# Performance work log

Measured on AMD Instinct MI355X. Metric: run time of the kernel, lower is better.

The kernel has to match this reference:

```python
import jax, jax.numpy as jnp
import numpy as np

B, C_IN, H, W = 2, 32, 512, 512
HIDDEN, SIZE = 768, 16
LATENT, NUM_CLASS = 128, 21
HP, WP = H // SIZE, W // SIZE
EPS = 1e-8
TEMP = 0.5


def setup_inputs() -> dict:
    key = jax.random.key(0)
    k1, k2, k3, k4, k5 = jax.random.split(key, 5)
    x = jax.random.normal(k1, (B, C_IN, H, W), dtype=jnp.float32)
    mask = jax.random.randint(k2, (B, NUM_CLASS, HP, WP), 0, 2).astype(jnp.int32)
    conv_w = jax.random.normal(k3, (HIDDEN, C_IN, SIZE, SIZE), dtype=jnp.float32) * 0.02
    conv_b = jax.random.normal(k4, (HIDDEN,), dtype=jnp.float32) * 0.02
    latent = jax.random.normal(k5, (1, LATENT * NUM_CLASS, HIDDEN), dtype=jnp.float32)
    return {"x": x, "mask": mask, "conv_w": conv_w, "conv_b": conv_b, "latent": latent}


def reference(x, mask, conv_w, conv_b, latent):
    # Patch embedding: Conv2d(kernel=stride=16) -> (B, HIDDEN, HP, WP)
    patch = jax.lax.conv_general_dilated(
        x, conv_w, window_strides=(SIZE, SIZE), padding='VALID',
        dimension_numbers=('NCHW', 'OIHW', 'NCHW'))
    patch = patch + conv_b[None, :, None, None]
    Bv = x.shape[0]
    N = HP * WP
    patch = patch.reshape(Bv, HIDDEN, N).transpose(0, 2, 1)  # (B, N, D)
    lat = jnp.broadcast_to(latent, (Bv, LATENT * NUM_CLASS, HIDDEN))  # (B, LC, D)

    # Cosine similarity as normalized batched matmul (same math as
    # torch CosineSimilarity over broadcast (B, LC, N, D))
    dots = jnp.einsum('bld,bnd->bln', lat, patch)  # (B, LC, N)
    lat_norm = jnp.linalg.norm(lat, axis=-1)       # (B, LC)
    pat_norm = jnp.linalg.norm(patch, axis=-1)     # (B, N)
    sim = dots / jnp.maximum(lat_norm[:, :, None] * pat_norm[:, None, :], EPS)

    sim = sim.reshape(Bv, LATENT, NUM_CLASS, HP, WP).mean(axis=1)  # (B, C, HP, WP)

    m = mask.astype(jnp.float32) >= 0.5
    s = jnp.sum(jnp.where(m, jnp.exp(sim / TEMP), 0.0))
    return -jnp.log(s)
```

## Files before the change

### kernel.cpp

```cpp
#include <hip/hip_runtime.h>
#include <math.h>

#define B_     2
#define CIN    32
#define HH     512
#define WW     512
#define HID    768
#define SZ     16
#define NPATCH 1024
#define KDIM   8192
#define NCLS   21
#define LAT    128
#define LC     2688
#define NP     (B_ * NPATCH)

#define NB_CL  63
#define NB_W4  1536
#define NB_XT  2048

typedef __attribute__((ext_vector_type(8))) short short8;
typedef __attribute__((ext_vector_type(4))) float f32x4;

__device__ __forceinline__ ushort f2bf(float f) {
    union { float f; unsigned u; } v; v.f = f;
    unsigned r = (v.u + 0x7fff + ((v.u >> 16) & 1)) >> 16;
    return (ushort)r;
}
__device__ __forceinline__ float bf2f(ushort u) {
    union { unsigned u; float f; } v; v.u = (unsigned)u << 16;
    return v.f;
}

__device__ __forceinline__ void gload16(const void* g, void* l) {
    __builtin_amdgcn_global_load_lds(
        (const __attribute__((address_space(1))) unsigned int*)g,
        (__attribute__((address_space(3))) unsigned int*)l, 16, 0, 0);
}

__global__ __launch_bounds__(256) void k_prep(const float* __restrict__ w,
                                              const float* __restrict__ x,
                                              const float* __restrict__ lat,
                                              ushort* __restrict__ wb,
                                              ushort* __restrict__ xb,
                                              float* __restrict__ classlat) {
    const int bid = blockIdx.x;
    const int t   = threadIdx.x;

    if (bid < NB_CL) {
        const int cls  = bid / 3;
        const int dseg = bid % 3;
        const int lane = t & 63, wvv = t >> 6;
        __shared__ float sc_sh[LAT];

        for (int q = 0; q < 32; q += 2) {
            int u0 = wvv * 32 + q;
            const float* r0 = lat + (size_t)(u0 * NCLS + cls) * HID;
            const float* r1 = lat + (size_t)((u0 + 1) * NCLS + cls) * HID;
            float s0 = 0.f, s1 = 0.f;
#pragma unroll
            for (int e = 0; e < HID / 64; ++e) {
                float a = r0[lane + e * 64]; s0 += a * a;
                float b2 = r1[lane + e * 64]; s1 += b2 * b2;
            }
#pragma unroll
            for (int off = 32; off >= 1; off >>= 1) {
                s0 += __shfl_xor(s0, off, 64);
                s1 += __shfl_xor(s1, off, 64);
            }
            if (lane == 0) {
                sc_sh[u0]     = 1.0f / (128.0f * sqrtf(s0));
                sc_sh[u0 + 1] = 1.0f / (128.0f * sqrtf(s1));
            }
        }
        __syncthreads();

        const float* src = lat + (size_t)cls * HID + dseg * 256 + t;
        float a = 0.f;
        for (int u0 = 0; u0 < LAT; u0 += 8) {
            float v[8];
#pragma unroll
            for (int q = 0; q < 8; ++q)
                v[q] = src[(size_t)(u0 + q) * (NCLS * HID)];
#pragma unroll
            for (int q = 0; q < 8; ++q) a += v[q] * sc_sh[u0 + q];
        }
        classlat[cls * HID + dseg * 256 + t] = a;
    } else if (bid < NB_CL + NB_W4) {
        const int cb = bid - NB_CL;
        float4 vv[4];
#pragma unroll
        for (int k = 0; k < 4; ++k)
            vv[k] = *(const float4*)(w + ((size_t)cb * 1024 + k * 256 + t) * 4);
#pragma unroll
        for (int k = 0; k < 4; ++k) {
            ushort4 o;
            o.x = f2bf(vv[k].x); o.y = f2bf(vv[k].y);
            o.z = f2bf(vv[k].z); o.w = f2bf(vv[k].w);
            *(ushort4*)(wb + ((size_t)cb * 1024 + k * 256 + t) * 4) = o;
        }
    } else {
        __shared__ ushort sh[32 * 264];
        const int cvb = bid - (NB_CL + NB_W4);
        const int c  = cvb >> 6;
        const int b  = (cvb >> 5) & 1;
        const int ph = cvb & 31;
        const float* src = x + (((size_t)(b * CIN + c) * HH) + (size_t)ph * 16) * WW;

        float4 vv[8];
#pragma unroll
        for (int q = 0; q < 8; ++q) {
            int f  = q * 256 + t;
            int i  = f >> 7;
            int w4 = f & 127;
            vv[q] = *(const float4*)(src + (size_t)i * WW + w4 * 4);
        }
#pragma unroll
        for (int q = 0; q < 8; ++q) {
            int f  = q * 256 + t;
            int i  = f >> 7;
            int w4 = f & 127;
            int pw = w4 >> 2, j0 = (w4 & 3) * 4;
            ushort4 o;
            o.x = f2bf(vv[q].x); o.y = f2bf(vv[q].y);
            o.z = f2bf(vv[q].z); o.w = f2bf(vv[q].w);
            *(ushort4*)&sh[pw * 264 + i * 16 + j0] = o;
        }
        __syncthreads();

        ushort* dst = xb + ((size_t)c * NP + b * 1024 + ph * 32) * 256;
        short8 rv[4];
#pragma unroll
        for (int q = 0; q < 4; ++q) {
            int s  = q * 256 + t;
            int pw = s >> 5;
            int o8 = (s & 31) * 8;
            rv[q] = *(const short8*)&sh[pw * 264 + o8];
        }
#pragma unroll
        for (int q = 0; q < 4; ++q)
            *(short8*)&dst[(size_t)(q * 256 + t) * 8] = rv[q];
    }
}

template <int SPLITK>
__global__ __launch_bounds__(512) void k_gemm(const ushort* __restrict__ xb,
                                              const ushort* __restrict__ wb,
                                              ushort* __restrict__ pbuf) {
    constexpr int KS = KDIM / SPLITK;
    __shared__ ushort Als[256 * 64];
    __shared__ ushort Bls[128 * 64];

    const int flat = blockIdx.x + 8 * (blockIdx.y + 6 * blockIdx.z);
    constexpr int nwg = 48 * SPLITK;
    const int wg = (flat & 7) * (nwg >> 3) + (flat >> 3);
    const int bz = wg / 48;
    const int rr = wg - bz * 48;
    const int by = rr % 6;
    const int bx = rr / 6;

    const int tid  = threadIdx.x;
    const int wv   = tid >> 6;
    const int lane = tid & 63;
    const int wm   = (wv >> 1) * 64;
    const int wn   = (wv & 1) * 64;

    const size_t bbase = ((size_t)by * 128) * KDIM + (size_t)bz * KS;

    const int srow  = wv * 8 + (lane >> 3);
    const int skoff = (((lane & 7) ^ (lane >> 3)) * 8);

    f32x4 acc[4][4];
#pragma unroll
    for (int m = 0; m < 4; ++m)
#pragma unroll
        for (int n = 0; n < 4; ++n) acc[m][n] = (f32x4)(0.f);

    const int fr = lane & 15, fq = lane >> 4;
    const int frx = (fr & 7) * 8;

    for (int kk = 0; kk < KS; kk += 64) {
        const int gk = bz * KS + kk;
        const size_t arow0 = (size_t)(gk >> 8) * NP + (size_t)bx * 256;
        const int ro = gk & 255;
#pragma unroll
        for (int q = 0; q < 4; ++q) {
            gload16(&xb[(arow0 + q * 64 + srow) * 256 + ro + skoff],
                    &Als[(q * 64 + wv * 8) * 64]);
        }
#pragma unroll
        for (int q = 0; q < 2; ++q) {
            const int row = q * 64 + srow;
            gload16(&wb[bbase + (size_t)row * KDIM + kk + skoff],
                    &Bls[(q * 64 + wv * 8) * 64]);
        }
        __syncthreads();

#pragma unroll
        for (int s = 0; s < 2; ++s) {
            short8 af[4], bf[4];
#pragma unroll
            for (int m = 0; m < 4; ++m)
                af[m] = *(const short8*)&Als[(wm + m * 16 + fr) * 64 + ((s * 32 + fq * 8) ^ frx)];
#pragma unroll
            for (int n = 0; n < 4; ++n)
                bf[n] = *(const short8*)&Bls[(wn + n * 16 + fr) * 64 + ((s * 32 + fq * 8) ^ frx)];
#pragma unroll
            for (int m = 0; m < 4; ++m)
#pragma unroll
                for (int n = 0; n < 4; ++n)
                    acc[m][n] = __builtin_amdgcn_mfma_f32_16x16x32_bf16(af[m], bf[n], acc[m][n], 0, 0, 0);
        }
        __syncthreads();
    }

#pragma unroll
    for (int m = 0; m < 4; ++m) {
#pragma unroll
        for (int n = 0; n < 4; ++n) {
            int col = by * 128 + wn + n * 16 + fr;
#pragma unroll
            for (int j = 0; j < 4; ++j) {
                int row = bx * 256 + wm + m * 16 + fq * 4 + j;
                pbuf[((size_t)row * SPLITK + bz) * HID + col] = f2bf(acc[m][n][j]);
            }
        }
    }
}

template <int SPLITK>
__global__ __launch_bounds__(256) void k_final(const ushort* __restrict__ pbuf,
                                               const float* __restrict__ conv_b,
                                               const float* __restrict__ classlat,
                                               const int* __restrict__ mask,
                                               float* __restrict__ partial) {
    const int p = blockIdx.x;
    const int b = p >> 10, n = p & 1023;
    const int t = threadIdx.x;
    const int lane = t & 63, wv = t >> 6;

    __shared__ ushort sh[SPLITK * HID];
    const ushort* pb = pbuf + (size_t)p * (SPLITK * HID);
    for (int i = t; i < SPLITK * HID / 8; i += 256)
        *(short8*)&sh[i * 8] = *(const short8*)&pb[(size_t)i * 8];
    __syncthreads();

    float f0 = conv_b[t], f1 = conv_b[t + 256], f2 = conv_b[t + 512];
#pragma unroll
    for (int z = 0; z < SPLITK; ++z) {
        f0 += bf2f(sh[z * HID + t]);
        f1 += bf2f(sh[z * HID + t + 256]);
        f2 += bf2f(sh[z * HID + t + 512]);
    }

    __shared__ float wsum[4];
    __shared__ float wdot[4][NCLS];
    __shared__ float cpart[NCLS];

    float ss = f0 * f0 + f1 * f1 + f2 * f2;
#pragma unroll
    for (int off = 32; off >= 1; off >>= 1) ss += __shfl_xor(ss, off, 64);
    if (lane == 0) wsum[wv] = ss;

    float dots[NCLS];
#pragma unroll
    for (int c = 0; c < NCLS; ++c) {
        const float* cl = classlat + c * HID;
        dots[c] = cl[t] * f0 + cl[t + 256] * f1 + cl[t + 512] * f2;
    }
#pragma unroll
    for (int c = 0; c < NCLS; ++c) {
        float v = dots[c];
#pragma unroll
        for (int off = 32; off >= 1; off >>= 1) v += __shfl_xor(v, off, 64);
        if (lane == 0) wdot[wv][c] = v;
    }
    __syncthreads();

    if (t < NCLS) {
        float tot  = wsum[0] + wsum[1] + wsum[2] + wsum[3];
        float invn = 1.0f / sqrtf(tot);
        float dot  = wdot[0][t] + wdot[1][t] + wdot[2][t] + wdot[3][t];
        float sim  = dot * invn;
        int   mv   = mask[(size_t)(b * NCLS + t) * NPATCH + n];
        cpart[t]   = (mv != 0) ? expf(sim * 2.0f) : 0.0f;
    }
    __syncthreads();
    if (t == 0) {
        float s = 0.f;
#pragma unroll
        for (int c = 0; c < NCLS; ++c) s += cpart[c];
        partial[p] = s;
    }
}

__global__ __launch_bounds__(256) void k_reduce(const float* __restrict__ partial,
                                                float* __restrict__ out) {
    int t = threadIdx.x;
    float s = 0.f;
    for (int i = t; i < NP; i += 256) s += partial[i];
#pragma unroll
    for (int off = 32; off >= 1; off >>= 1) s += __shfl_xor(s, off, 64);
    __shared__ float ws[4];
    if ((t & 63) == 0) ws[t >> 6] = s;
    __syncthreads();
    if (t == 0) out[0] = -logf(ws[0] + ws[1] + ws[2] + ws[3]);
}

extern "C" void kernel_launch(void* const* d_in, const int* in_sizes, int n_in,
                              void* d_out, int out_size, void* d_ws, size_t ws_size,
                              hipStream_t stream) {
    const float* x      = (const float*)d_in[0];
    const int*   mask   = (const int*)d_in[1];
    const float* conv_w = (const float*)d_in[2];
    const float* conv_b = (const float*)d_in[3];
    const float* latent = (const float*)d_in[4];
    float* out = (float*)d_out;

    const size_t xb_bytes   = (size_t)NP * KDIM * 2;
    const size_t wb_bytes   = (size_t)HID * KDIM * 2;
    const size_t pslice     = (size_t)NP * HID * 2;
    const size_t small_need = (size_t)NCLS * HID * 4 + NP * 4 + 256;

    char* base = (char*)d_ws;
    ushort* xb   = (ushort*)base;
    ushort* wb   = (ushort*)(base + xb_bytes);
    ushort* pbuf = (ushort*)(base + xb_bytes + wb_bytes);

    int splitk = 1;
    const size_t fixed = xb_bytes + wb_bytes + small_need;
    if (ws_size >= fixed + 8 * pslice)      splitk = 8;
    else if (ws_size >= fixed + 4 * pslice) splitk = 4;
    else if (ws_size >= fixed + 2 * pslice) splitk = 2;

    float* classlat = (float*)(base + xb_bytes + wb_bytes + (size_t)splitk * pslice);
    float* partial  = classlat + NCLS * HID;

    k_prep<<<NB_CL + NB_W4 + NB_XT, 256, 0, stream>>>(conv_w, x, latent,
                                                      wb, xb, classlat);

    dim3 g(NP / 256, HID / 128, splitk);
    switch (splitk) {
        case 8: k_gemm<8><<<g, 512, 0, stream>>>(xb, wb, pbuf); break;
        case 4: k_gemm<4><<<g, 512, 0, stream>>>(xb, wb, pbuf); break;
        case 2: k_gemm<2><<<g, 512, 0, stream>>>(xb, wb, pbuf); break;
        default: k_gemm<1><<<g, 512, 0, stream>>>(xb, wb, pbuf); break;
    }

    switch (splitk) {
        case 8: k_final<8><<<NP, 256, 0, stream>>>(pbuf, conv_b, classlat, mask, partial); break;
        case 4: k_final<4><<<NP, 256, 0, stream>>>(pbuf, conv_b, classlat, mask, partial); break;
        case 2: k_final<2><<<NP, 256, 0, stream>>>(pbuf, conv_b, classlat, mask, partial); break;
        default: k_final<1><<<NP, 256, 0, stream>>>(pbuf, conv_b, classlat, mask, partial); break;
    }
    k_reduce<<<1, 256, 0, stream>>>(partial, out);
}
```

Before: 86.31 us.

## Fuse input im2col and bf16 conversion into GEMM A-tile loading

Removes the separate pass that converted x to a bf16 patch-major buffer and instead has the GEMM read fp32 x directly, convert to bf16 in registers and scatter into a padded LDS tile. This is meant to eliminate a 32 MB bf16 write plus reread and the extra prep blocks. In exchange, A loads become synchronous register loads rather than async global-to-LDS copies, and each block reads fp32 data, twice the bytes per element. The XOR swizzle on A is replaced by padding to a stride of 72.

```diff
diff --git a/kernel.cpp b/kernel.cpp
--- a/kernel.cpp
+++ b/kernel.cpp
@@ -1,4 +1,5 @@
 #include <hip/hip_runtime.h>
+#include <hip/hip_bf16.h>
 #include <math.h>
 
 #define B_     2
@@ -16,7 +17,6 @@
 
 #define NB_CL  63
 #define NB_W4  1536
-#define NB_XT  2048
 
 typedef __attribute__((ext_vector_type(8))) short short8;
 typedef __attribute__((ext_vector_type(4))) float f32x4;
@@ -37,11 +37,15 @@
         (__attribute__((address_space(3))) unsigned int*)l, 16, 0, 0);
 }
 
+__device__ __forceinline__ unsigned pk2bf(float a, float b) {
+    union { __hip_bfloat162 h; unsigned u; } cv;
+    cv.h = __float22bfloat162_rn(make_float2(a, b));
+    return cv.u;
+}
+
 __global__ __launch_bounds__(256) void k_prep(const float* __restrict__ w,
-                                              const float* __restrict__ x,
                                               const float* __restrict__ lat,
                                               ushort* __restrict__ wb,
-                                              ushort* __restrict__ xb,
                                               float* __restrict__ classlat) {
     const int bid = blockIdx.x;
     const int t   = threadIdx.x;
@@ -85,7 +89,7 @@
             for (int q = 0; q < 8; ++q) a += v[q] * sc_sh[u0 + q];
         }
         classlat[cls * HID + dseg * 256 + t] = a;
-    } else if (bid < NB_CL + NB_W4) {
+    } else {
         const int cb = bid - NB_CL;
         float4 vv[4];
 #pragma unroll
@@ -98,56 +102,15 @@
             o.z = f2bf(vv[k].z); o.w = f2bf(vv[k].w);
             *(ushort4*)(wb + ((size_t)cb * 1024 + k * 256 + t) * 4) = o;
         }
-    } else {
-        __shared__ ushort sh[32 * 264];
-        const int cvb = bid - (NB_CL + NB_W4);
-        const int c  = cvb >> 6;
-        const int b  = (cvb >> 5) & 1;
-        const int ph = cvb & 31;
-        const float* src = x + (((size_t)(b * CIN + c) * HH) + (size_t)ph * 16) * WW;
-
-        float4 vv[8];
-#pragma unroll
-        for (int q = 0; q < 8; ++q) {
-            int f  = q * 256 + t;
-            int i  = f >> 7;
-            int w4 = f & 127;
-            vv[q] = *(const float4*)(src + (size_t)i * WW + w4 * 4);
-        }
-#pragma unroll
-        for (int q = 0; q < 8; ++q) {
-            int f  = q * 256 + t;
-            int i  = f >> 7;
-            int w4 = f & 127;
-            int pw = w4 >> 2, j0 = (w4 & 3) * 4;
-            ushort4 o;
-            o.x = f2bf(vv[q].x); o.y = f2bf(vv[q].y);
-            o.z = f2bf(vv[q].z); o.w = f2bf(vv[q].w);
-            *(ushort4*)&sh[pw * 264 + i * 16 + j0] = o;
-        }
-        __syncthreads();
-
-        ushort* dst = xb + ((size_t)c * NP + b * 1024 + ph * 32) * 256;
-        short8 rv[4];
-#pragma unroll
-        for (int q = 0; q < 4; ++q) {
-            int s  = q * 256 + t;
-            int pw = s >> 5;
-            int o8 = (s & 31) * 8;
-            rv[q] = *(const short8*)&sh[pw * 264 + o8];
-        }
-#pragma unroll
-        for (int q = 0; q < 4; ++q)
-            *(short8*)&dst[(size_t)(q * 256 + t) * 8] = rv[q];
     }
 }
 
 template <int SPLITK>
-__global__ __launch_bounds__(512) void k_gemm(const ushort* __restrict__ xb,
+__global__ __launch_bounds__(512) void k_gemm(const float* __restrict__ x,
                                               const ushort* __restrict__ wb,
                                               ushort* __restrict__ pbuf) {
     constexpr int KS = KDIM / SPLITK;
-    __shared__ ushort Als[256 * 64];
+    __shared__ ushort Als[256 * 72];
     __shared__ ushort Bls[128 * 64];
 
     const int flat = blockIdx.x + 8 * (blockIdx.y + 6 * blockIdx.z);
@@ -164,6 +127,9 @@
     const int wm   = (wv >> 1) * 64;
     const int wn   = (wv & 1) * 64;
 
+    const int bxb = bx >> 2;
+    const int ph0 = (bx & 3) * 8;
+
     const size_t bbase = ((size_t)by * 128) * KDIM + (size_t)bz * KS;
 
     const int srow  = wv * 8 + (lane >> 3);
@@ -180,12 +146,18 @@
 
     for (int kk = 0; kk < KS; kk += 64) {
         const int gk = bz * KS + kk;
-        const size_t arow0 = (size_t)(gk >> 8) * NP + (size_t)bx * 256;
-        const int ro = gk & 255;
-#pragma unroll
-        for (int q = 0; q < 4; ++q) {
-            gload16(&xb[(arow0 + q * 64 + srow) * 256 + ro + skoff],
-                    &Als[(q * 64 + wv * 8) * 64]);
+        const int c  = gk >> 8;
+        const int i0 = (gk >> 4) & 15;
+        const float* xA = x + (((size_t)(bxb * CIN + c) * HH) + ph0 * 16 + i0) * WW;
+
+        float4 vv[8];
+#pragma unroll
+        for (int q = 0; q < 8; ++q) {
+            int f    = q * 512 + tid;
+            int row5 = f >> 7;
+            int w4   = f & 127;
+            vv[q] = *(const float4*)(xA + (size_t)((row5 >> 2) * 16 + (row5 & 3)) * WW
+                                        + w4 * 4);
         }
 #pragma unroll
         for (int q = 0; q < 2; ++q) {
@@ -193,6 +165,18 @@
             gload16(&wb[bbase + (size_t)row * KDIM + kk + skoff],
                     &Bls[(q * 64 + wv * 8) * 64]);
         }
+#pragma unroll
+        for (int q = 0; q < 8; ++q) {
+            int f    = q * 512 + tid;
+            int row5 = f >> 7;
+            int w4   = f & 127;
+            int r    = ((row5 >> 2) << 5) + (w4 >> 2);
+            int e    = ((row5 & 3) << 4) + ((w4 & 3) << 2);
+            uint2 o;
+            o.x = pk2bf(vv[q].x, vv[q].y);
+            o.y = pk2bf(vv[q].z, vv[q].w);
+            *(uint2*)&Als[r * 72 + e] = o;
+        }
         __syncthreads();
 
 #pragma unroll
@@ -200,7 +184,7 @@
             short8 af[4], bf[4];
 #pragma unroll
             for (int m = 0; m < 4; ++m)
-                af[m] = *(const short8*)&Als[(wm + m * 16 + fr) * 64 + ((s * 32 + fq * 8) ^ frx)];
+                af[m] = *(const short8*)&Als[(wm + m * 16 + fr) * 72 + s * 32 + fq * 8];
 #pragma unroll
             for (int n = 0; n < 4; ++n)
                 bf[n] = *(const short8*)&Bls[(wn + n * 16 + fr) * 64 + ((s * 32 + fq * 8) ^ frx)];
@@ -316,34 +300,31 @@
     const float* latent = (const float*)d_in[4];
     float* out = (float*)d_out;
 
-    const size_t xb_bytes   = (size_t)NP * KDIM * 2;
     const size_t wb_bytes   = (size_t)HID * KDIM * 2;
     const size_t pslice     = (size_t)NP * HID * 2;
     const size_t small_need = (size_t)NCLS * HID * 4 + NP * 4 + 256;
 
     char* base = (char*)d_ws;
-    ushort* xb   = (ushort*)base;
-    ushort* wb   = (ushort*)(base + xb_bytes);
-    ushort* pbuf = (ushort*)(base + xb_bytes + wb_bytes);
+    ushort* wb   = (ushort*)base;
+    ushort* pbuf = (ushort*)(base + wb_bytes);
 
     int splitk = 1;
-    const size_t fixed = xb_bytes + wb_bytes + small_need;
+    const size_t fixed = wb_bytes + small_need;
     if (ws_size >= fixed + 8 * pslice)      splitk = 8;
     else if (ws_size >= fixed + 4 * pslice) splitk = 4;
     else if (ws_size >= fixed + 2 * pslice) splitk = 2;
 
-    float* classlat = (float*)(base + xb_bytes + wb_bytes + (size_t)splitk * pslice);
+    float* classlat = (float*)(base + wb_bytes + (size_t)splitk * pslice);
     float* partial  = classlat + NCLS * HID;
 
-    k_prep<<<NB_CL + NB_W4 + NB_XT, 256, 0, stream>>>(conv_w, x, latent,
-                                                      wb, xb, classlat);
+    k_prep<<<NB_CL + NB_W4, 256, 0, stream>>>(conv_w, latent, wb, classlat);
 
     dim3 g(NP / 256, HID / 128, splitk);
     switch (splitk) {
-        case 8: k_gemm<8><<<g, 512, 0, stream>>>(xb, wb, pbuf); break;
-        case 4: k_gemm<4><<<g, 512, 0, stream>>>(xb, wb, pbuf); break;
-        case 2: k_gemm<2><<<g, 512, 0, stream>>>(xb, wb, pbuf); break;
-        default: k_gemm<1><<<g, 512, 0, stream>>>(xb, wb, pbuf); break;
+        case 8: k_gemm<8><<<g, 512, 0, stream>>>(x, wb, pbuf); break;
+        case 4: k_gemm<4><<<g, 512, 0, stream>>>(x, wb, pbuf); break;
+        case 2: k_gemm<2><<<g, 512, 0, stream>>>(x, wb, pbuf); break;
+        default: k_gemm<1><<<g, 512, 0, stream>>>(x, wb, pbuf); break;
     }
 
     switch (splitk) {
```

Measured after the change: 103.5 us. +19.9%, slower.
